# Kernel optimization log

Measured on AMD Instinct MI355X. Metric: run time of the kernel, lower is better.

Reference implementation:

```python
import jax, jax.numpy as jnp
import numpy as np

T, B, D = 512, 16, 1024  # time-major [T, B, D], D = 2*hid_dim
WIN = 16                 # attn_winsize


def setup_inputs() -> dict:
    key = jax.random.key(0)
    k1, k2 = jax.random.split(key)
    x = jax.random.normal(k1, (T, B, D), dtype=jnp.float32)
    # scorer: nn.Linear(2*D, 1) -> weight [2*D], bias [1]
    w = jax.random.normal(k2, (2 * D,), dtype=jnp.float32) * (1.0 / np.sqrt(2 * D))
    b = jnp.zeros((1,), dtype=jnp.float32)
    return {"x": x, "w": w, "b": b, "win_size": WIN}


def reference(x, w, b, win_size):
    # Faithful vectorization of getAttnOutput: for each timestep i, the window is
    # softmax over window positions (per batch element); weighted sum over window.
    Tn, Bn, Dn = x.shape
    w_cur, w_seq = w[:Dn], w[Dn:]
    a = jnp.einsum('tbd,d->tb', x, w_cur)   # query-side score term  [T, B]
    c = jnp.einsum('tbd,d->tb', x, w_seq)   # key-side score term    [T, B]

    offs = jnp.arange(-win_size, win_size + 1)            # [W]
    idx = jnp.arange(Tn)[:, None] + offs[None, :]         # [T, W]
    valid = (idx >= 0) & (idx < Tn)                       # [T, W]
    idxc = jnp.clip(idx, 0, Tn - 1)

    scores = a[:, None, :] + c[idxc] + b[0]               # [T, W, B]
    scores = jnp.where(valid[:, :, None], scores, -jnp.inf)
    p = jax.nn.softmax(scores, axis=1)                    # softmax over window dim

    windows = x[idxc]                                     # [T, W, B, D] (gather)
    attn = jnp.einsum('twb,twbd->tbd', p, windows)        # [T, B, D]
    return jnp.concatenate([x, attn], axis=2)             # [T, B, 2D]
```

## Files before the change

kernel.cpp:

```cpp
#include <hip/hip_runtime.h>

#define T_DIM 512
#define B_DIM 16
#define D_DIM 1024
#define WINR  16
#define NW    33
#define TT    16
#define NR    (TT + 2 * WINR)

typedef float f32x2 __attribute__((ext_vector_type(2)));
typedef float f32x4 __attribute__((ext_vector_type(4)));

__global__ __launch_bounds__(256) void calc_c_kernel(const float* __restrict__ x,
                                                     const float* __restrict__ w,
                                                     float* __restrict__ c) {
    const int wave = threadIdx.x >> 6;
    const int lane = threadIdx.x & 63;
    const int pair = blockIdx.x * 4 + wave;
    const f32x4* x4 = reinterpret_cast<const f32x4*>(x + (size_t)pair * D_DIM);
    const f32x4* w4 = reinterpret_cast<const f32x4*>(w + D_DIM);
    float acc = 0.f;
    #pragma unroll
    for (int i = 0; i < 4; ++i) {
        f32x4 xv = x4[i * 64 + lane];
        f32x4 wv = w4[i * 64 + lane];
        acc += xv.x * wv.x + xv.y * wv.y + xv.z * wv.z + xv.w * wv.w;
    }
    #pragma unroll
    for (int off = 32; off; off >>= 1) acc += __shfl_xor(acc, off, 64);
    if (lane == 0) c[pair] = acc;
}

__global__ __launch_bounds__(256) void attn_kernel(const float* __restrict__ x,
                                                   const float* __restrict__ c,
                                                   float* __restrict__ out) {
    __shared__ __align__(16) float dd[NR][TT];

    const int half = blockIdx.x & 1;
    const int b    = (blockIdx.x >> 1) & (B_DIM - 1);
    const int t0   = (blockIdx.x >> 5) * TT;
    const int tid  = threadIdx.x;
    const int d0   = half * (D_DIM / 2) + tid * 2;
    const size_t rs = (size_t)B_DIM * D_DIM;

    {
        float* ddf = &dd[0][0];
        #pragma unroll
        for (int i = 0; i < (NR * TT) / 256; ++i) ddf[tid + i * 256] = 0.f;
    }
    __syncthreads();

    if (tid < TT) {
        const int t = t0 + tid;
        float sc[NW];
        float m = -1e30f;
        #pragma unroll
        for (int ww = 0; ww < NW; ++ww) {
            const int s = t - WINR + ww;
            const float v = (s >= 0 && s < T_DIM) ? c[s * B_DIM + b] : -1e30f;
            sc[ww] = v;
            m = fmaxf(m, v);
        }
        float sum = 0.f;
        #pragma unroll
        for (int ww = 0; ww < NW; ++ww) {
            const float e = (sc[ww] > -1e29f) ? __expf(sc[ww] - m) : 0.f;
            sc[ww] = e;
            sum += e;
        }
        const float inv = 1.f / sum;
        #pragma unroll
        for (int ww = 0; ww < NW; ++ww) dd[tid + ww][tid] = sc[ww] * inv;
    }
    __syncthreads();

    f32x2 acc[TT];
    #pragma unroll
    for (int j = 0; j < TT; ++j) acc[j] = (f32x2){0.f, 0.f};

    const float* xb = x + (size_t)b * D_DIM + d0;
    float* ob = out + (size_t)b * 2 * D_DIM + d0;

    #pragma unroll 2
    for (int ss = -WINR; ss < TT + WINR; ++ss) {
        const int s = t0 + ss;
        f32x2 xs = (f32x2){0.f, 0.f};
        if ((unsigned)s < (unsigned)T_DIM) {
            xs = *reinterpret_cast<const f32x2*>(xb + (size_t)s * rs);
        }
        if ((unsigned)ss < (unsigned)TT) {
            *reinterpret_cast<f32x2*>(ob + (size_t)(t0 + ss) * 2 * rs) = xs;
        }
        const f32x4* dr = reinterpret_cast<const f32x4*>(dd[ss + WINR]);
        const f32x4 q0 = dr[0], q1 = dr[1], q2 = dr[2], q3 = dr[3];

        #define FMA2(j, pv) \
            acc[j].x += (pv) * xs.x; acc[j].y += (pv) * xs.y;
        FMA2(0,  q0.x) FMA2(1,  q0.y) FMA2(2,  q0.z) FMA2(3,  q0.w)
        FMA2(4,  q1.x) FMA2(5,  q1.y) FMA2(6,  q1.z) FMA2(7,  q1.w)
        FMA2(8,  q2.x) FMA2(9,  q2.y) FMA2(10, q2.z) FMA2(11, q2.w)
        FMA2(12, q3.x) FMA2(13, q3.y) FMA2(14, q3.z) FMA2(15, q3.w)
        #undef FMA2
    }

    #pragma unroll
    for (int j = 0; j < TT; ++j) {
        *reinterpret_cast<f32x2*>(ob + (size_t)(t0 + j) * 2 * rs + D_DIM) = acc[j];
    }
}

extern "C" void kernel_launch(void* const* d_in, const int* in_sizes, int n_in,
                              void* d_out, int out_size, void* d_ws, size_t ws_size,
                              hipStream_t stream) {
    const float* x = (const float*)d_in[0];
    const float* w = (const float*)d_in[1];
    float* c   = (float*)d_ws;
    float* out = (float*)d_out;

    calc_c_kernel<<<(T_DIM * B_DIM) / 4, 256, 0, stream>>>(x, w, c);
    attn_kernel<<<(T_DIM / TT) * B_DIM * 2, 256, 0, stream>>>(x, c, out);
}
```

Baseline: 113.0 us.

## Double time tile and split D into quarters with scalar loads and row prefetch

Doubles the per-block time tile to 32 and splits the feature dimension into four quarters with one float per thread, which lowers the halo re-read ratio for the sliding window. It also software-prefetches the next input row before the FMA work. The trade-off is 32 accumulators per thread, more registers, and a softmax computed by more threads per block.

```diff
diff --git a/kernel.cpp b/kernel.cpp
--- a/kernel.cpp
+++ b/kernel.cpp
@@ -5,10 +5,10 @@
 #define D_DIM 1024
 #define WINR  16
 #define NW    33
-#define TT    16
+#define TT    32
 #define NR    (TT + 2 * WINR)
+#define DQ    256
 
-typedef float f32x2 __attribute__((ext_vector_type(2)));
 typedef float f32x4 __attribute__((ext_vector_type(4)));
 
 __global__ __launch_bounds__(256) void calc_c_kernel(const float* __restrict__ x,
@@ -36,12 +36,12 @@
                                                    float* __restrict__ out) {
     __shared__ __align__(16) float dd[NR][TT];
 
-    const int half = blockIdx.x & 1;
-    const int b    = (blockIdx.x >> 1) & (B_DIM - 1);
-    const int t0   = (blockIdx.x >> 5) * TT;
-    const int tid  = threadIdx.x;
-    const int d0   = half * (D_DIM / 2) + tid * 2;
-    const size_t rs = (size_t)B_DIM * D_DIM;
+    const int q   = blockIdx.x & 3;
+    const int b   = (blockIdx.x >> 2) & (B_DIM - 1);
+    const int t0  = (blockIdx.x >> 6) * TT;
+    const int tid = threadIdx.x;
+    const size_t rs  = (size_t)B_DIM * D_DIM;
+    const size_t ros = (size_t)B_DIM * 2 * D_DIM;
 
     {
         float* ddf = &dd[0][0];
@@ -74,38 +74,45 @@
     }
     __syncthreads();
 
-    f32x2 acc[TT];
+    float acc[TT];
     #pragma unroll
-    for (int j = 0; j < TT; ++j) acc[j] = (f32x2){0.f, 0.f};
+    for (int j = 0; j < TT; ++j) acc[j] = 0.f;
 
-    const float* xb = x + (size_t)b * D_DIM + d0;
-    float* ob = out + (size_t)b * 2 * D_DIM + d0;
+    const float* xb = x + (size_t)b * D_DIM + q * DQ + tid;
+    float* ob = out + (size_t)b * 2 * D_DIM + q * DQ + tid;
 
+    auto loadrow = [&](int s) -> float {
+        return ((unsigned)s < (unsigned)T_DIM) ? xb[(size_t)s * rs] : 0.f;
+    };
+
+    float xs = loadrow(t0 - WINR);
     #pragma unroll 2
     for (int ss = -WINR; ss < TT + WINR; ++ss) {
-        const int s = t0 + ss;
-        f32x2 xs = (f32x2){0.f, 0.f};
-        if ((unsigned)s < (unsigned)T_DIM) {
-            xs = *reinterpret_cast<const f32x2*>(xb + (size_t)s * rs);
-        }
+        const float xn = loadrow(t0 + ss + 1);
         if ((unsigned)ss < (unsigned)TT) {
-            *reinterpret_cast<f32x2*>(ob + (size_t)(t0 + ss) * 2 * rs) = xs;
+            ob[(size_t)(t0 + ss) * ros] = xs;
         }
         const f32x4* dr = reinterpret_cast<const f32x4*>(dd[ss + WINR]);
-        const f32x4 q0 = dr[0], q1 = dr[1], q2 = dr[2], q3 = dr[3];
 
-        #define FMA2(j, pv) \
-            acc[j].x += (pv) * xs.x; acc[j].y += (pv) * xs.y;
-        FMA2(0,  q0.x) FMA2(1,  q0.y) FMA2(2,  q0.z) FMA2(3,  q0.w)
-        FMA2(4,  q1.x) FMA2(5,  q1.y) FMA2(6,  q1.z) FMA2(7,  q1.w)
-        FMA2(8,  q2.x) FMA2(9,  q2.y) FMA2(10, q2.z) FMA2(11, q2.w)
-        FMA2(12, q3.x) FMA2(13, q3.y) FMA2(14, q3.z) FMA2(15, q3.w)
-        #undef FMA2
+        #define FMA8(base, qq) \
+            acc[base + 0] += (qq).x * xs; acc[base + 1] += (qq).y * xs; \
+            acc[base + 2] += (qq).z * xs; acc[base + 3] += (qq).w * xs;
+        {
+            const f32x4 q0 = dr[0], q1 = dr[1], q2 = dr[2], q3 = dr[3];
+            FMA8(0, q0) FMA8(4, q1) FMA8(8, q2) FMA8(12, q3)
+        }
+        {
+            const f32x4 q4 = dr[4], q5 = dr[5], q6 = dr[6], q7 = dr[7];
+            FMA8(16, q4) FMA8(20, q5) FMA8(24, q6) FMA8(28, q7)
+        }
+        #undef FMA8
+
+        xs = xn;
     }
 
     #pragma unroll
     for (int j = 0; j < TT; ++j) {
-        *reinterpret_cast<f32x2*>(ob + (size_t)(t0 + j) * 2 * rs + D_DIM) = acc[j];
+        ob[(size_t)(t0 + j) * ros + D_DIM] = acc[j];
     }
 }
 
@@ -118,5 +125,5 @@
     float* out = (float*)d_out;
 
     calc_c_kernel<<<(T_DIM * B_DIM) / 4, 256, 0, stream>>>(x, w, c);
-    attn_kernel<<<(T_DIM / TT) * B_DIM * 2, 256, 0, stream>>>(x, c, out);
+    attn_kernel<<<(T_DIM / TT) * B_DIM * 4, 256, 0, stream>>>(x, c, out);
 }
```

Measured after the change: 120.4 us. +6.6%, slower.
